# Kernel tuning notes

Measured on AMD Instinct MI355X. Metric: run time of the kernel, lower is better.

## Reference

```python
import jax, jax.numpy as jnp
import numpy as np

B, T, D = 2, 2048, 2048
H, HD = 16, 128          # n_heads, head_dim
K, L = 4, 24             # n_bases, total_layers
FF = D * 1               # ff_mult = 1 (required by route_down dim match)


def setup_inputs() -> dict:
    key = jax.random.key(0)
    ks = jax.random.split(key, 16)
    s = jnp.float32(0.02)
    bias_base = jnp.zeros((L, K), jnp.float32).at[:, 0].set(5.0)
    return {
        "x": jax.random.normal(ks[0], (B, T, D), jnp.float32),
        "gamma": jnp.ones((D,), jnp.float32),
        "beta": jnp.zeros((D,), jnp.float32),
        "iter_scale": jnp.ones((), jnp.float32),
        "qkv_bases": jax.random.normal(ks[1], (K, 3 * D, D), jnp.float32) * s,
        "o_bases": jax.random.normal(ks[2], (K, D, D), jnp.float32) * s,
        "gate_bases": jax.random.normal(ks[3], (K, FF, D), jnp.float32) * s,
        "up_bases": jax.random.normal(ks[4], (K, FF, D), jnp.float32) * s,
        "down_bases": jax.random.normal(ks[5], (K, D, FF), jnp.float32) * s,
        "route_qkv": jax.random.normal(ks[6], (L, K, D), jnp.float32) * s,
        "route_o": jax.random.normal(ks[7], (L, K, D), jnp.float32) * s,
        "route_gate": jax.random.normal(ks[8], (L, K, D), jnp.float32) * s,
        "route_up": jax.random.normal(ks[9], (L, K, D), jnp.float32) * s,
        "route_down": jax.random.normal(ks[10], (L, K, FF), jnp.float32) * s,
        "bias_qkv": bias_base + 0.1 * jax.random.normal(ks[11], (L, K), jnp.float32),
        "bias_o": bias_base + 0.1 * jax.random.normal(ks[12], (L, K), jnp.float32),
        "bias_gate": bias_base + 0.1 * jax.random.normal(ks[13], (L, K), jnp.float32),
        "bias_up": bias_base + 0.1 * jax.random.normal(ks[14], (L, K), jnp.float32),
        "bias_down": bias_base + 0.1 * jax.random.normal(ks[15], (L, K), jnp.float32),
        "norm1_w": jnp.ones((D,), jnp.float32),
        "norm2_w": jnp.ones((D,), jnp.float32),
        "layer_idx": 5,
    }


def _rmsnorm(x, w):
    eps = jnp.finfo(x.dtype).eps  # nn.RMSNorm default eps
    return x * jax.lax.rsqrt(jnp.mean(x * x, axis=-1, keepdims=True) + eps) * w


def _mixed_linear(x, bases, route_l, bias_l):
    # route_l: (K, d_in), bias_l: (K,) for this layer
    logits = jnp.einsum('btd,kd->btk', x, route_l) / jnp.sqrt(jnp.float32(D)) + bias_l
    alpha = jax.nn.softmax(logits, axis=-1)                    # (B,T,K)
    y = jnp.einsum('btk,kod,btd->bto', alpha, bases, x)        # weighted combine of K linears
    return y, alpha


def reference(x, gamma, beta, iter_scale, qkv_bases, o_bases, gate_bases, up_bases,
              down_bases, route_qkv, route_o, route_gate, route_up, route_down,
              bias_qkv, bias_o, bias_gate, bias_up, bias_down, norm1_w, norm2_w, layer_idx):
    li = layer_idx
    h = _rmsnorm(x, norm1_w) * gamma + beta
    qkv, a_qkv = _mixed_linear(h, qkv_bases, route_qkv[li], bias_qkv[li])
    qkv = qkv.reshape(B, T, 3, H, HD).transpose(2, 0, 3, 1, 4)  # (3,B,H,T,HD)
    q, k, v = qkv[0], qkv[1], qkv[2]
    scores = jnp.einsum('bhqd,bhkd->bhqk', q, k) / jnp.sqrt(jnp.float32(HD))
    causal = jnp.triu(jnp.ones((T, T), bool), 1)
    scores = jnp.where(causal, -jnp.inf, scores)
    attn = jax.nn.softmax(scores, axis=-1)
    out = jnp.einsum('bhqk,bhkd->bhqd', attn, v).transpose(0, 2, 1, 3).reshape(B, T, D)
    attn_out, _ = _mixed_linear(out, o_bases, route_o[li], bias_o[li])
    x_attn = x + attn_out
    h2 = _rmsnorm(x_attn, norm2_w) * gamma + beta
    gate_out, _ = _mixed_linear(h2, gate_bases, route_gate[li], bias_gate[li])
    up_out, _ = _mixed_linear(h2, up_bases, route_up[li], bias_up[li])
    ffn_in = jax.nn.silu(gate_out) * up_out
    down_out, _ = _mixed_linear(ffn_in, down_bases, route_down[li], bias_down[li])
    x_ffn = x_attn + down_out
    return x + (x_ffn - x) * iter_scale, a_qkv
```

## Files before the change

kernel.cpp:

```cpp
#include <hip/hip_runtime.h>


typedef __attribute__((ext_vector_type(8))) short short8;
typedef __attribute__((ext_vector_type(4))) float f32x4;
typedef __attribute__((ext_vector_type(4))) unsigned uint4_t;

#define BT 4096
#define DD 2048
#define KD 8192
#define NH 16
#define HD_ 128
#define RSCALE 0.02209708691207961f
#define ASCALE 0.08838834764831845f

__device__ inline float bf2f(short s) {
  return __uint_as_float(((unsigned)(unsigned short)s) << 16);
}
__device__ inline short f2bf(float f) {
  unsigned u = __float_as_uint(f);
  u += 0x7FFFu + ((u >> 16) & 1u);
  return (short)(u >> 16);
}
__device__ inline f32x4 zero4() { f32x4 v; v[0]=0.f; v[1]=0.f; v[2]=0.f; v[3]=0.f; return v; }

__device__ inline void async_copy16(const void* g, void* l) {
  __builtin_amdgcn_global_load_lds(
      (const __attribute__((address_space(1))) unsigned*)g,
      (__attribute__((address_space(3))) unsigned*)l, 16, 0, 0);
}

__global__ __launch_bounds__(256)
void cvt_bf16_kernel(const float* __restrict__ in, short* __restrict__ out,
                     const int nchunk) {
  const int i = blockIdx.x * 256 + threadIdx.x;
  if (i >= nchunk) return;
  const float* p = in + (size_t)i * 8;
  float4 u0 = *(const float4*)p;
  float4 u1 = *(const float4*)(p + 4);
  uint4_t pk;
  pk[0] = __builtin_amdgcn_perm(__float_as_uint(u0.y), __float_as_uint(u0.x), 0x07060302);
  pk[1] = __builtin_amdgcn_perm(__float_as_uint(u0.w), __float_as_uint(u0.z), 0x07060302);
  pk[2] = __builtin_amdgcn_perm(__float_as_uint(u1.y), __float_as_uint(u1.x), 0x07060302);
  pk[3] = __builtin_amdgcn_perm(__float_as_uint(u1.w), __float_as_uint(u1.z), 0x07060302);
  *(uint4_t*)(out + (size_t)i * 8) = pk;
}

__global__ __launch_bounds__(256)
void rmsnorm_kernel(const float* __restrict__ x, const float* __restrict__ w,
                    const float* __restrict__ gamma, const float* __restrict__ beta,
                    short* __restrict__ out) {
  const int t = blockIdx.x;
  const float* xr = x + (size_t)t * DD;
  const int base = threadIdx.x * 8;
  float4 v0 = *(const float4*)(xr + base);
  float4 v1 = *(const float4*)(xr + base + 4);
  float ss = v0.x*v0.x + v0.y*v0.y + v0.z*v0.z + v0.w*v0.w
           + v1.x*v1.x + v1.y*v1.y + v1.z*v1.z + v1.w*v1.w;
  #pragma unroll
  for (int off = 32; off > 0; off >>= 1) ss += __shfl_xor(ss, off, 64);
  __shared__ float red[4];
  const int lane = threadIdx.x & 63, wv = threadIdx.x >> 6;
  if (lane == 0) red[wv] = ss;
  __syncthreads();
  const float tot = red[0] + red[1] + red[2] + red[3];
  const float inv = rsqrtf(tot * (1.0f / DD) + 1.1920929e-07f);
  float xv[8] = {v0.x,v0.y,v0.z,v0.w,v1.x,v1.y,v1.z,v1.w};
  short8 o;
  #pragma unroll
  for (int j = 0; j < 8; ++j)
    o[j] = f2bf(xv[j] * inv * w[base+j] * gamma[base+j] + beta[base+j]);
  *(short8*)(out + (size_t)t * DD + base) = o;
}

__global__ __launch_bounds__(64)
void route_kernel(const short* __restrict__ in,
                  const float* __restrict__ routeB,
                  const float* __restrict__ biasB,
                  const int* __restrict__ li_ptr,
                  float* __restrict__ alpha,
                  float* __restrict__ aout)
{
  const int t = blockIdx.x;
  const int lane = threadIdx.x;
  const int li = *li_ptr;
  const float* R = routeB + (size_t)li * 4 * DD;
  const float* bias = biasB + li * 4;
  const short* xr = in + (size_t)t * DD;
  float acc0 = 0.f, acc1 = 0.f, acc2 = 0.f, acc3 = 0.f;
  for (int i = lane; i < DD; i += 64) {
    float v = bf2f(xr[i]);
    acc0 += v * R[i];
    acc1 += v * R[DD + i];
    acc2 += v * R[2*DD + i];
    acc3 += v * R[3*DD + i];
  }
  #pragma unroll
  for (int off = 32; off > 0; off >>= 1) {
    acc0 += __shfl_xor(acc0, off, 64);
    acc1 += __shfl_xor(acc1, off, 64);
    acc2 += __shfl_xor(acc2, off, 64);
    acc3 += __shfl_xor(acc3, off, 64);
  }
  if (lane == 0) {
    float lg[4] = {acc0 * RSCALE + bias[0], acc1 * RSCALE + bias[1],
                   acc2 * RSCALE + bias[2], acc3 * RSCALE + bias[3]};
    float mx = fmaxf(fmaxf(lg[0], lg[1]), fmaxf(lg[2], lg[3]));
    float se = 0.f;
    #pragma unroll
    for (int k = 0; k < 4; ++k) { lg[k] = __expf(lg[k] - mx); se += lg[k]; }
    const float rinv = 1.0f / se;
    #pragma unroll
    for (int k = 0; k < 4; ++k) {
      float a = lg[k] * rinv;
      alpha[(size_t)t*4 + k] = a;
      if (aout) aout[(size_t)t*4 + k] = a;
    }
  }
}

__global__ __launch_bounds__(256)
void expand_kernel(const short* __restrict__ in, const float* __restrict__ alpha,
                   short* __restrict__ out)
{
  const int t = blockIdx.x;
  const short* hr = in + (size_t)t * DD;
  const float a0 = alpha[(size_t)t*4], a1 = alpha[(size_t)t*4+1],
              a2 = alpha[(size_t)t*4+2], a3 = alpha[(size_t)t*4+3];
  const float av[4] = {a0, a1, a2, a3};
  #pragma unroll
  for (int c = 0; c < 4; ++c) {
    int ci = threadIdx.x + 256 * c;
    int kk = ci * 8;
    int kidx = kk >> 11;
    int d = kk & 2047;
    short8 v = *(const short8*)(hr + d);
    float s = av[kidx];
    short8 o;
    #pragma unroll
    for (int j = 0; j < 8; ++j) o[j] = f2bf(bf2f(v[j]) * s);
    *(short8*)(out + (size_t)t * KD + kk) = o;
  }
}

__global__ __launch_bounds__(256)
void gemm_qkv(const short* __restrict__ Aexp,
              const short* __restrict__ Bwb,
              short* __restrict__ outp)
{
  __shared__ __align__(16) short As[128*64];
  __shared__ __align__(16) short Bs[128*64];
  const int tid = threadIdx.x;
  const int lane = tid & 63, wave = tid >> 6;
  const int lr = lane & 15, lg = lane >> 4;
  const int wm = (wave & 1) * 64, wn = (wave >> 1) * 64;
  const int m0 = blockIdx.y * 128, n0 = blockIdx.x * 128;

  f32x4 acc[4][4];
  #pragma unroll
  for (int i = 0; i < 4; ++i)
    #pragma unroll
    for (int j = 0; j < 4; ++j) acc[i][j] = zero4();

  const int srow = tid >> 3, sc8 = tid & 7;
  const short* Ab = Aexp + (size_t)(m0 + srow) * KD + sc8 * 8;
  const short* Bb = Bwb + (size_t)(n0 + srow) * DD + sc8 * 8;

  for (int kt = 0; kt < 128; ++kt) {
    const int kk0 = kt << 6;
    const int kidx = kk0 >> 11;
    const int dbase = kk0 & 2047;
    #pragma unroll
    for (int c = 0; c < 4; ++c) {
      const int i = tid + 256 * c;
      async_copy16(Ab + (size_t)(c * 32) * KD + kk0, As + i * 8);
      async_copy16(Bb + ((size_t)kidx * 6144 + c * 32) * DD + dbase, Bs + i * 8);
    }
    __syncthreads();
    #pragma unroll
    for (int s = 0; s < 2; ++s) {
      short8 af[4], bfr[4];
      #pragma unroll
      for (int i = 0; i < 4; ++i) af[i]  = *(const short8*)(As + (wm + i*16 + lr)*64 + s*32 + lg*8);
      #pragma unroll
      for (int j = 0; j < 4; ++j) bfr[j] = *(const short8*)(Bs + (wn + j*16 + lr)*64 + s*32 + lg*8);
      #pragma unroll
      for (int i = 0; i < 4; ++i)
        #pragma unroll
        for (int j = 0; j < 4; ++j)
          acc[i][j] = __builtin_amdgcn_mfma_f32_16x16x32_bf16(af[i], bfr[j], acc[i][j], 0, 0, 0);
    }
    __syncthreads();
  }
  #pragma unroll
  for (int i = 0; i < 4; ++i) {
    #pragma unroll
    for (int r = 0; r < 4; ++r) {
      const int m = m0 + wm + i*16 + lg*4 + r;
      #pragma unroll
      for (int j = 0; j < 4; ++j) {
        const int n = n0 + wn + j*16 + lr;
        outp[(size_t)m * 6144 + n] = f2bf(acc[i][j][r]);
      }
    }
  }
}

__global__ __launch_bounds__(256)
void gemm_wide(const short* __restrict__ A,
               const short* __restrict__ Bc,
               short* __restrict__ Z)
{
  __shared__ __align__(16) short As[128*64];
  __shared__ __align__(16) short Bs[128*64];
  const int tid = threadIdx.x;
  const int lane = tid & 63, wave = tid >> 6;
  const int lr = lane & 15, lg = lane >> 4;
  const int wm = (wave & 1) * 64, wn = (wave >> 1) * 64;
  const int m0 = blockIdx.y * 128, n0 = blockIdx.x * 128;

  f32x4 acc[4][4];
  #pragma unroll
  for (int i = 0; i < 4; ++i)
    #pragma unroll
    for (int j = 0; j < 4; ++j) acc[i][j] = zero4();

  const int srow = tid >> 3, sc8 = tid & 7;
  const short* Ab = A  + (size_t)(m0 + srow) * DD + sc8 * 8;
  const short* Bb = Bc + (size_t)(n0 + srow) * DD + sc8 * 8;

  for (int kt = 0; kt < 32; ++kt) {
    const int kk0 = kt << 6;
    #pragma unroll
    for (int c = 0; c < 4; ++c) {
      const int i = tid + 256 * c;
      async_copy16(Ab + (size_t)(c * 32) * DD + kk0, As + i * 8);
      async_copy16(Bb + (size_t)(c * 32) * DD + kk0, Bs + i * 8);
    }
    __syncthreads();
    #pragma unroll
    for (int s = 0; s < 2; ++s) {
      short8 af[4], bfr[4];
      #pragma unroll
      for (int i = 0; i < 4; ++i) af[i]  = *(const short8*)(As + (wm + i*16 + lr)*64 + s*32 + lg*8);
      #pragma unroll
      for (int j = 0; j < 4; ++j) bfr[j] = *(const short8*)(Bs + (wn + j*16 + lr)*64 + s*32 + lg*8);
      #pragma unroll
      for (int i = 0; i < 4; ++i)
        #pragma unroll
        for (int j = 0; j < 4; ++j)
          acc[i][j] = __builtin_amdgcn_mfma_f32_16x16x32_bf16(af[i], bfr[j], acc[i][j], 0, 0, 0);
    }
    __syncthreads();
  }
  #pragma unroll
  for (int i = 0; i < 4; ++i) {
    #pragma unroll
    for (int r = 0; r < 4; ++r) {
      const int m = m0 + wm + i*16 + lg*4 + r;
      #pragma unroll
      for (int j = 0; j < 4; ++j) {
        const int n = n0 + wn + j*16 + lr;
        Z[(size_t)m * 8192 + n] = f2bf(acc[i][j][r]);
      }
    }
  }
}

__global__ __launch_bounds__(256)
void combine_kernel(const short* __restrict__ Z,
                    const float* __restrict__ alpha,
                    const int mode,
                    const float* __restrict__ x,
                    const float* __restrict__ xattn,
                    const float* __restrict__ iter_s,
                    const short* __restrict__ gate,
                    void* __restrict__ outp)
{
  const int t = blockIdx.x;
  const int d0 = threadIdx.x * 8;
  const float a0 = alpha[(size_t)t*4],   a1 = alpha[(size_t)t*4+1],
              a2 = alpha[(size_t)t*4+2], a3 = alpha[(size_t)t*4+3];
  const short* zr = Z + (size_t)t * 8192 + d0;
  short8 z0 = *(const short8*)(zr);
  short8 z1 = *(const short8*)(zr + 2048);
  short8 z2 = *(const short8*)(zr + 4096);
  short8 z3 = *(const short8*)(zr + 6144);
  float y[8];
  #pragma unroll
  for (int j = 0; j < 8; ++j)
    y[j] = a0*bf2f(z0[j]) + a1*bf2f(z1[j]) + a2*bf2f(z2[j]) + a3*bf2f(z3[j]);
  const size_t base = (size_t)t * DD + d0;
  if (mode == 0) {
    short8 o;
    #pragma unroll
    for (int j = 0; j < 8; ++j) o[j] = f2bf(y[j]);
    *(short8*)((short*)outp + base) = o;
  } else if (mode == 1) {
    float4 x0 = *(const float4*)(x + base);
    float4 x1 = *(const float4*)(x + base + 4);
    float xv[8] = {x0.x,x0.y,x0.z,x0.w,x1.x,x1.y,x1.z,x1.w};
    float* op = (float*)outp;
    #pragma unroll
    for (int j = 0; j < 8; ++j) op[base + j] = xv[j] + y[j];
  } else if (mode == 2) {
    short8 gv = *(const short8*)(gate + base);
    short8 o;
    #pragma unroll
    for (int j = 0; j < 8; ++j) {
      float xg = bf2f(gv[j]);
      float s = xg / (1.0f + __expf(-xg));
      o[j] = f2bf(s * y[j]);
    }
    *(short8*)((short*)outp + base) = o;
  } else {
    const float is = *iter_s;
    float4 x0 = *(const float4*)(x + base);
    float4 x1 = *(const float4*)(x + base + 4);
    float4 t0 = *(const float4*)(xattn + base);
    float4 t1 = *(const float4*)(xattn + base + 4);
    float xv[8] = {x0.x,x0.y,x0.z,x0.w,x1.x,x1.y,x1.z,x1.w};
    float tv[8] = {t0.x,t0.y,t0.z,t0.w,t1.x,t1.y,t1.z,t1.w};
    float* op = (float*)outp;
    #pragma unroll
    for (int j = 0; j < 8; ++j) op[base + j] = xv[j] + (tv[j] + y[j] - xv[j]) * is;
  }
}

__global__ __launch_bounds__(256)
void transpose_v_kernel(const short* __restrict__ qkv, short* __restrict__ vt)
{
  __shared__ __align__(16) short tile[64][72];
  const int t0 = blockIdx.x * 64;
  const int hd0 = blockIdx.y * 64;
  const int bh = blockIdx.z;
  const int b = bh >> 4, h = bh & 15;
  const int tid = threadIdx.x;
  #pragma unroll
  for (int c = 0; c < 2; ++c) {
    int ci = tid + 256 * c;
    int tr = ci >> 3, c8 = ci & 7;
    *(short8*)&tile[tr][c8*8] =
      *(const short8*)(qkv + (size_t)(b*2048 + t0 + tr)*6144 + 4096 + h*HD_ + hd0 + c8*8);
  }
  __syncthreads();
  #pragma unroll
  for (int c = 0; c < 2; ++c) {
    int ci = tid + 256 * c;
    int hr = ci >> 3, c8 = ci & 7;
    short8 o;
    #pragma unroll
    for (int j = 0; j < 8; ++j) o[j] = tile[c8*8 + j][hr];
    *(short8*)(vt + (size_t)(bh*HD_ + hd0 + hr)*2048 + t0 + c8*8) = o;
  }
}

__global__ __launch_bounds__(256, 2)
void attn_kernel(const short* __restrict__ qkv,
                 const short* __restrict__ vt,
                 short* __restrict__ attnout)
{
  __shared__ __align__(16) short Ks[32][136];
  __shared__ __align__(16) short Vt[128][40];
  __shared__ __align__(16) short Ps[4][16][40];
  const int bid = blockIdx.x;
  const int qt = bid & 31, bh = bid >> 5;
  const int b = bh >> 4, h = bh & 15;
  const int q0 = qt * 64;
  const int tid = threadIdx.x, lane = tid & 63, w = tid >> 6;
  const int lr = lane & 15, lg = lane >> 4;
  const int q0w = q0 + w * 16;

  short8 qf[4];
  {
    const size_t qbase = (size_t)(b*2048 + q0w + lr) * 6144 + h * HD_;
    #pragma unroll
    for (int s = 0; s < 4; ++s)
      qf[s] = *(const short8*)(qkv + qbase + s*32 + lg*8);
  }
  float m_run[4], l_run[4];
  f32x4 acc[8];
  #pragma unroll
  for (int r = 0; r < 4; ++r) { m_run[r] = -1e30f; l_run[r] = 0.f; }
  #pragma unroll
  for (int dt = 0; dt < 8; ++dt) acc[dt] = zero4();

  const int ntiles = (q0 + 64) >> 5;
  for (int jt = 0; jt < ntiles; ++jt) {
    const int j0 = jt << 5;
    #pragma unroll
    for (int c = 0; c < 2; ++c) {
      int ci = tid + 256 * c;
      int key = ci >> 4, hd8 = ci & 15;
      *(short8*)&Ks[key][hd8*8] =
        *(const short8*)(qkv + (size_t)(b*2048 + j0 + key)*6144 + 2048 + h*HD_ + hd8*8);
    }
    #pragma unroll
    for (int c = 0; c < 2; ++c) {
      int ci = tid + 256 * c;
      int hd = ci >> 2, k8 = ci & 3;
      *(short8*)&Vt[hd][k8*8] =
        *(const short8*)(vt + (size_t)(bh*HD_ + hd)*2048 + j0 + k8*8);
    }
    __syncthreads();
    f32x4 sc0 = zero4(), sc1 = zero4();
    #pragma unroll
    for (int s = 0; s < 4; ++s) {
      short8 kb0 = *(const short8*)&Ks[lr][s*32 + lg*8];
      short8 kb1 = *(const short8*)&Ks[16 + lr][s*32 + lg*8];
      sc0 = __builtin_amdgcn_mfma_f32_16x16x32_bf16(qf[s], kb0, sc0, 0, 0, 0);
      sc1 = __builtin_amdgcn_mfma_f32_16x16x32_bf16(qf[s], kb1, sc1, 0, 0, 0);
    }
    float pv0[4], pv1[4], al[4];
    #pragma unroll
    for (int r = 0; r < 4; ++r) {
      const int q = q0w + lg*4 + r;
      float v0 = sc0[r] * ASCALE; if (j0 + lr > q)      v0 = -1e30f;
      float v1 = sc1[r] * ASCALE; if (j0 + 16 + lr > q) v1 = -1e30f;
      float mx = fmaxf(v0, v1);
      mx = fmaxf(mx, __shfl_xor(mx, 1, 16));
      mx = fmaxf(mx, __shfl_xor(mx, 2, 16));
      mx = fmaxf(mx, __shfl_xor(mx, 4, 16));
      mx = fmaxf(mx, __shfl_xor(mx, 8, 16));
      const float mnew = fmaxf(m_run[r], mx);
      const float a = __expf(m_run[r] - mnew);
      v0 = __expf(v0 - mnew);
      v1 = __expf(v1 - mnew);
      float rs = v0 + v1;
      rs += __shfl_xor(rs, 1, 16);
      rs += __shfl_xor(rs, 2, 16);
      rs += __shfl_xor(rs, 4, 16);
      rs += __shfl_xor(rs, 8, 16);
      l_run[r] = l_run[r] * a + rs;
      m_run[r] = mnew;
      al[r] = a; pv0[r] = v0; pv1[r] = v1;
    }
    #pragma unroll
    for (int dt = 0; dt < 8; ++dt)
      #pragma unroll
      for (int r = 0; r < 4; ++r) acc[dt][r] *= al[r];
    #pragma unroll
    for (int r = 0; r < 4; ++r) {
      Ps[w][lg*4 + r][lr]      = f2bf(pv0[r]);
      Ps[w][lg*4 + r][16 + lr] = f2bf(pv1[r]);
    }
    short8 pa = *(const short8*)&Ps[w][lr][lg*8];
    #pragma unroll
    for (int dt = 0; dt < 8; ++dt) {
      short8 vb = *(const short8*)&Vt[dt*16 + lr][lg*8];
      acc[dt] = __builtin_amdgcn_mfma_f32_16x16x32_bf16(pa, vb, acc[dt], 0, 0, 0);
    }
    __syncthreads();
  }
  #pragma unroll
  for (int dt = 0; dt < 8; ++dt) {
    #pragma unroll
    for (int r = 0; r < 4; ++r) {
      const int q = q0w + lg*4 + r;
      attnout[(size_t)(b*2048 + q)*2048 + h*HD_ + dt*16 + lr] = f2bf(acc[dt][r] / l_run[r]);
    }
  }
}

extern "C" void kernel_launch(void* const* d_in, const int* in_sizes, int n_in,
                              void* d_out, int out_size, void* d_ws, size_t ws_size,
                              hipStream_t stream) {
  const float* x          = (const float*)d_in[0];
  const float* gamma      = (const float*)d_in[1];
  const float* beta       = (const float*)d_in[2];
  const float* iter_scale = (const float*)d_in[3];
  const float* qkv_bases  = (const float*)d_in[4];
  const float* o_bases    = (const float*)d_in[5];
  const float* gate_bases = (const float*)d_in[6];
  const float* up_bases   = (const float*)d_in[7];
  const float* down_bases = (const float*)d_in[8];
  const float* route_qkv  = (const float*)d_in[9];
  const float* route_o    = (const float*)d_in[10];
  const float* route_gate = (const float*)d_in[11];
  const float* route_up   = (const float*)d_in[12];
  const float* route_down = (const float*)d_in[13];
  const float* bias_qkv   = (const float*)d_in[14];
  const float* bias_o     = (const float*)d_in[15];
  const float* bias_gate  = (const float*)d_in[16];
  const float* bias_up    = (const float*)d_in[17];
  const float* bias_down  = (const float*)d_in[18];
  const float* norm1_w    = (const float*)d_in[19];
  const float* norm2_w    = (const float*)d_in[20];
  const int*   li         = (const int*)d_in[21];

  float* out0 = (float*)d_out;
  float* aout = out0 + (size_t)BT * DD;

  char* ws = (char*)d_ws;
  short* hbuf    = (short*)(ws + 0);
  float* alpha   = (float*)(ws + 16777216);
  short* Zbuf    = (short*)(ws + 16842752);
  short* Bconv   = (short*)(ws + 83951616);
  short* qkvbuf  = (short*)(ws + 184614912);
  short* vtbuf   = (short*)(ws + 234946560);
  short* attnout = (short*)(ws + 251723776);
  float* x_attn  = (float*)(ws + 184614912);
  short* gatebuf = (short*)(ws + 218169344);

  const int NCH_QKV = 50331648 / 8;
  const int NCH_D   = 16777216 / 8;

  rmsnorm_kernel<<<BT, 256, 0, stream>>>(x, norm1_w, gamma, beta, hbuf);
  cvt_bf16_kernel<<<NCH_QKV/256, 256, 0, stream>>>(qkv_bases, Bconv, NCH_QKV);
  route_kernel<<<BT, 64, 0, stream>>>(hbuf, route_qkv, bias_qkv, li, alpha, aout);
  expand_kernel<<<BT, 256, 0, stream>>>(hbuf, alpha, Zbuf);
  gemm_qkv<<<dim3(48, 32), 256, 0, stream>>>(Zbuf, Bconv, qkvbuf);
  transpose_v_kernel<<<dim3(32, 2, 32), 256, 0, stream>>>(qkvbuf, vtbuf);
  attn_kernel<<<1024, 256, 0, stream>>>(qkvbuf, vtbuf, attnout);
  cvt_bf16_kernel<<<NCH_D/256, 256, 0, stream>>>(o_bases, Bconv, NCH_D);
  route_kernel<<<BT, 64, 0, stream>>>(attnout, route_o, bias_o, li, alpha, nullptr);
  gemm_wide<<<dim3(64, 32), 256, 0, stream>>>(attnout, Bconv, Zbuf);
  combine_kernel<<<BT, 256, 0, stream>>>(Zbuf, alpha, 1, x, nullptr, nullptr,
                                         nullptr, x_attn);
  rmsnorm_kernel<<<BT, 256, 0, stream>>>(x_attn, norm2_w, gamma, beta, hbuf);
  cvt_bf16_kernel<<<NCH_D/256, 256, 0, stream>>>(gate_bases, Bconv, NCH_D);
  route_kernel<<<BT, 64, 0, stream>>>(hbuf, route_gate, bias_gate, li, alpha, nullptr);
  gemm_wide<<<dim3(64, 32), 256, 0, stream>>>(hbuf, Bconv, Zbuf);
  combine_kernel<<<BT, 256, 0, stream>>>(Zbuf, alpha, 0, nullptr, nullptr, nullptr,
                                         nullptr, gatebuf);
  cvt_bf16_kernel<<<NCH_D/256, 256, 0, stream>>>(up_bases, Bconv, NCH_D);
  route_kernel<<<BT, 64, 0, stream>>>(hbuf, route_up, bias_up, li, alpha, nullptr);
  gemm_wide<<<dim3(64, 32), 256, 0, stream>>>(hbuf, Bconv, Zbuf);
  combine_kernel<<<BT, 256, 0, stream>>>(Zbuf, alpha, 2, nullptr, nullptr, nullptr,
                                         gatebuf, gatebuf);
  cvt_bf16_kernel<<<NCH_D/256, 256, 0, stream>>>(down_bases, Bconv, NCH_D);
  route_kernel<<<BT, 64, 0, stream>>>(gatebuf, route_down, bias_down, li, alpha, nullptr);
  gemm_wide<<<dim3(64, 32), 256, 0, stream>>>(gatebuf, Bconv, Zbuf);
  combine_kernel<<<BT, 256, 0, stream>>>(Zbuf, alpha, 3, x, x_attn, iter_scale,
                                         nullptr, out0);
}
```

Baseline: 1.996 ms.

## Replace GEMMs with 256x256-tile triple-buffered swizzled 8-wave MFMA kernel

Replaces the two 128x128 single-buffered GEMM kernels with one templated 512-thread kernel. It uses 256x256 output tiles and a 3-stage async-copy LDS ring with explicit vmcnt waits. An XOR swizzle on the LDS layout avoids bank conflicts, and setprio is raised around the MFMA block. The aim is to overlap global loads with compute, raise data reuse per tile and cut LDS conflicts. In exchange it uses more registers (32 accumulators per wave) and launches fewer blocks, which may hurt occupancy and tail balance.

```diff
diff --git a/kernel.cpp b/kernel.cpp
--- a/kernel.cpp
+++ b/kernel.cpp
@@ -142,128 +142,99 @@
   }
 }
 
-__global__ __launch_bounds__(256)
-void gemm_qkv(const short* __restrict__ Aexp,
-              const short* __restrict__ Bwb,
-              short* __restrict__ outp)
+__global__ __launch_bounds__(512)
+void gemm8p_qkv(const short* __restrict__ A, const short* __restrict__ B,
+                short* __restrict__ C);
+
+template<bool QKV, int AST, int KTOT, int NST>
+__global__ __launch_bounds__(512)
+void gemm8p(const short* __restrict__ A, const short* __restrict__ B,
+            short* __restrict__ C)
 {
-  __shared__ __align__(16) short As[128*64];
-  __shared__ __align__(16) short Bs[128*64];
+  constexpr int NS = KTOT / 32;
+  __shared__ __align__(16) short As[3][256 * 32];
+  __shared__ __align__(16) short Bs[3][256 * 32];
   const int tid = threadIdx.x;
   const int lane = tid & 63, wave = tid >> 6;
   const int lr = lane & 15, lg = lane >> 4;
-  const int wm = (wave & 1) * 64, wn = (wave >> 1) * 64;
-  const int m0 = blockIdx.y * 128, n0 = blockIdx.x * 128;
-
-  f32x4 acc[4][4];
-  #pragma unroll
-  for (int i = 0; i < 4; ++i)
+  const int wm = wave >> 2, wn = wave & 3;
+  const int m0 = blockIdx.y * 256, n0 = blockIdx.x * 256;
+
+  const int srow = tid >> 2;
+  const int pc = (tid & 3) ^ ((tid >> 3) & 3);
+  const short* Aab = A + (size_t)(m0 + srow) * AST + pc * 8;
+  const short* Bab = B + (size_t)(n0 + srow) * 2048 + pc * 8;
+
+  f32x4 acc[8][4];
+  #pragma unroll
+  for (int i = 0; i < 8; ++i)
     #pragma unroll
     for (int j = 0; j < 4; ++j) acc[i][j] = zero4();
 
-  const int srow = tid >> 3, sc8 = tid & 7;
-  const short* Ab = Aexp + (size_t)(m0 + srow) * KD + sc8 * 8;
-  const short* Bb = Bwb + (size_t)(n0 + srow) * DD + sc8 * 8;
-
-  for (int kt = 0; kt < 128; ++kt) {
-    const int kk0 = kt << 6;
-    const int kidx = kk0 >> 11;
-    const int dbase = kk0 & 2047;
-    #pragma unroll
-    for (int c = 0; c < 4; ++c) {
-      const int i = tid + 256 * c;
-      async_copy16(Ab + (size_t)(c * 32) * KD + kk0, As + i * 8);
-      async_copy16(Bb + ((size_t)kidx * 6144 + c * 32) * DD + dbase, Bs + i * 8);
-    }
-    __syncthreads();
-    #pragma unroll
-    for (int s = 0; s < 2; ++s) {
-      short8 af[4], bfr[4];
+  auto stage = [&](int ks_) {
+    const int b_ = ks_ % 3;
+    short* la = &As[b_][0] + tid * 8;
+    short* lb = &Bs[b_][0] + tid * 8;
+    if constexpr (QKV) {
+      const int kidx = ks_ >> 6;
+      const int dbase = (ks_ & 63) * 32;
+      const short* as_ = Aab + ks_ * 32;
+      const short* bs_ = Bab + (size_t)kidx * (6144 * 2048) + dbase;
+      async_copy16(as_, la);
+      async_copy16(as_ + 128 * AST, la + 4096);
+      async_copy16(bs_, lb);
+      async_copy16(bs_ + 128 * 2048, lb + 4096);
+    } else {
+      const int k0 = ks_ * 32;
+      async_copy16(Aab + k0, la);
+      async_copy16(Aab + k0 + 128 * AST, la + 4096);
+      async_copy16(Bab + k0, lb);
+      async_copy16(Bab + k0 + 128 * 2048, lb + 4096);
+    }
+  };
+
+  stage(0); stage(1); stage(2);
+
+  const int acol = (lg ^ ((lr >> 1) & 3)) * 8;
+
+  for (int ks = 0; ks < NS; ++ks) {
+    const int b = ks % 3;
+    const int rem = NS - 1 - ks;
+    if (rem >= 2)      asm volatile("s_waitcnt vmcnt(8)" ::: "memory");
+    else if (rem == 1) asm volatile("s_waitcnt vmcnt(4)" ::: "memory");
+    else               asm volatile("s_waitcnt vmcnt(0)" ::: "memory");
+    __builtin_amdgcn_s_barrier();
+    short8 af[8], bg[4];
+    const short* ap = &As[b][0] + (wm * 128 + lr) * 32 + acol;
+    #pragma unroll
+    for (int i = 0; i < 8; ++i) af[i] = *(const short8*)(ap + i * 512);
+    const short* bp = &Bs[b][0] + (wn * 64 + lr) * 32 + acol;
+    #pragma unroll
+    for (int j = 0; j < 4; ++j) bg[j] = *(const short8*)(bp + j * 512);
+    asm volatile("s_waitcnt lgkmcnt(0)" ::: "memory");
+    __builtin_amdgcn_sched_barrier(0);
+    __builtin_amdgcn_s_setprio(1);
+    #pragma unroll
+    for (int i = 0; i < 8; ++i)
       #pragma unroll
-      for (int i = 0; i < 4; ++i) af[i]  = *(const short8*)(As + (wm + i*16 + lr)*64 + s*32 + lg*8);
-      #pragma unroll
-      for (int j = 0; j < 4; ++j) bfr[j] = *(const short8*)(Bs + (wn + j*16 + lr)*64 + s*32 + lg*8);
-      #pragma unroll
-      for (int i = 0; i < 4; ++i)
-        #pragma unroll
-        for (int j = 0; j < 4; ++j)
-          acc[i][j] = __builtin_amdgcn_mfma_f32_16x16x32_bf16(af[i], bfr[j], acc[i][j], 0, 0, 0);
-    }
-    __syncthreads();
-  }
-  #pragma unroll
-  for (int i = 0; i < 4; ++i) {
+      for (int j = 0; j < 4; ++j)
+        acc[i][j] = __builtin_amdgcn_mfma_f32_16x16x32_bf16(af[i], bg[j], acc[i][j], 0, 0, 0);
+    __builtin_amdgcn_s_setprio(0);
+    __builtin_amdgcn_s_barrier();
+    if (ks + 3 < NS) stage(ks + 3);
+  }
+
+  #pragma unroll
+  for (int i = 0; i < 8; ++i)
     #pragma unroll
     for (int r = 0; r < 4; ++r) {
-      const int m = m0 + wm + i*16 + lg*4 + r;
+      const int m = m0 + wm * 128 + i * 16 + lg * 4 + r;
       #pragma unroll
       for (int j = 0; j < 4; ++j) {
-        const int n = n0 + wn + j*16 + lr;
-        outp[(size_t)m * 6144 + n] = f2bf(acc[i][j][r]);
+        const int n = n0 + wn * 64 + j * 16 + lr;
+        C[(size_t)m * NST + n] = f2bf(acc[i][j][r]);
       }
     }
-  }
-}
-
-__global__ __launch_bounds__(256)
-void gemm_wide(const short* __restrict__ A,
-               const short* __restrict__ Bc,
-               short* __restrict__ Z)
-{
-  __shared__ __align__(16) short As[128*64];
-  __shared__ __align__(16) short Bs[128*64];
-  const int tid = threadIdx.x;
-  const int lane = tid & 63, wave = tid >> 6;
-  const int lr = lane & 15, lg = lane >> 4;
-  const int wm = (wave & 1) * 64, wn = (wave >> 1) * 64;
-  const int m0 = blockIdx.y * 128, n0 = blockIdx.x * 128;
-
-  f32x4 acc[4][4];
-  #pragma unroll
-  for (int i = 0; i < 4; ++i)
-    #pragma unroll
-    for (int j = 0; j < 4; ++j) acc[i][j] = zero4();
-
-  const int srow = tid >> 3, sc8 = tid & 7;
-  const short* Ab = A  + (size_t)(m0 + srow) * DD + sc8 * 8;
-  const short* Bb = Bc + (size_t)(n0 + srow) * DD + sc8 * 8;
-
-  for (int kt = 0; kt < 32; ++kt) {
-    const int kk0 = kt << 6;
-    #pragma unroll
-    for (int c = 0; c < 4; ++c) {
-      const int i = tid + 256 * c;
-      async_copy16(Ab + (size_t)(c * 32) * DD + kk0, As + i * 8);
-      async_copy16(Bb + (size_t)(c * 32) * DD + kk0, Bs + i * 8);
-    }
-    __syncthreads();
-    #pragma unroll
-    for (int s = 0; s < 2; ++s) {
-      short8 af[4], bfr[4];
-      #pragma unroll
-      for (int i = 0; i < 4; ++i) af[i]  = *(const short8*)(As + (wm + i*16 + lr)*64 + s*32 + lg*8);
-      #pragma unroll
-      for (int j = 0; j < 4; ++j) bfr[j] = *(const short8*)(Bs + (wn + j*16 + lr)*64 + s*32 + lg*8);
-      #pragma unroll
-      for (int i = 0; i < 4; ++i)
-        #pragma unroll
-        for (int j = 0; j < 4; ++j)
-          acc[i][j] = __builtin_amdgcn_mfma_f32_16x16x32_bf16(af[i], bfr[j], acc[i][j], 0, 0, 0);
-    }
-    __syncthreads();
-  }
-  #pragma unroll
-  for (int i = 0; i < 4; ++i) {
-    #pragma unroll
-    for (int r = 0; r < 4; ++r) {
-      const int m = m0 + wm + i*16 + lg*4 + r;
-      #pragma unroll
-      for (int j = 0; j < 4; ++j) {
-        const int n = n0 + wn + j*16 + lr;
-        Z[(size_t)m * 8192 + n] = f2bf(acc[i][j][r]);
-      }
-    }
-  }
 }
 
 __global__ __launch_bounds__(256)
@@ -508,28 +479,28 @@
   cvt_bf16_kernel<<<NCH_QKV/256, 256, 0, stream>>>(qkv_bases, Bconv, NCH_QKV);
   route_kernel<<<BT, 64, 0, stream>>>(hbuf, route_qkv, bias_qkv, li, alpha, aout);
   expand_kernel<<<BT, 256, 0, stream>>>(hbuf, alpha, Zbuf);
-  gemm_qkv<<<dim3(48, 32), 256, 0, stream>>>(Zbuf, Bconv, qkvbuf);
+  gemm8p<true, 8192, 8192, 6144><<<dim3(24, 16), 512, 0, stream>>>(Zbuf, Bconv, qkvbuf);
   transpose_v_kernel<<<dim3(32, 2, 32), 256, 0, stream>>>(qkvbuf, vtbuf);
   attn_kernel<<<1024, 256, 0, stream>>>(qkvbuf, vtbuf, attnout);
   cvt_bf16_kernel<<<NCH_D/256, 256, 0, stream>>>(o_bases, Bconv, NCH_D);
   route_kernel<<<BT, 64, 0, stream>>>(attnout, route_o, bias_o, li, alpha, nullptr);
-  gemm_wide<<<dim3(64, 32), 256, 0, stream>>>(attnout, Bconv, Zbuf);
+  gemm8p<false, 2048, 2048, 8192><<<dim3(32, 16), 512, 0, stream>>>(attnout, Bconv, Zbuf);
   combine_kernel<<<BT, 256, 0, stream>>>(Zbuf, alpha, 1, x, nullptr, nullptr,
                                          nullptr, x_attn);
   rmsnorm_kernel<<<BT, 256, 0, stream>>>(x_attn, norm2_w, gamma, beta, hbuf);
   cvt_bf16_kernel<<<NCH_D/256, 256, 0, stream>>>(gate_bases, Bconv, NCH_D);
   route_kernel<<<BT, 64, 0, stream>>>(hbuf, route_gate, bias_gate, li, alpha, nullptr);
-  gemm_wide<<<dim3(64, 32), 256, 0, stream>>>(hbuf, Bconv, Zbuf);
+  gemm8p<false, 2048, 2048, 8192><<<dim3(32, 16), 512, 0, stream>>>(hbuf, Bconv, Zbuf);
   combine_kernel<<<BT, 256, 0, stream>>>(Zbuf, alpha, 0, nullptr, nullptr, nullptr,
                                          nullptr, gatebuf);
   cvt_bf16_kernel<<<NCH_D/256, 256, 0, stream>>>(up_bases, Bconv, NCH_D);
   route_kernel<<<BT, 64, 0, stream>>>(hbuf, route_up, bias_up, li, alpha, nullptr);
-  gemm_wide<<<dim3(64, 32), 256, 0, stream>>>(hbuf, Bconv, Zbuf);
+  gemm8p<false, 2048, 2048, 8192><<<dim3(32, 16), 512, 0, stream>>>(hbuf, Bconv, Zbuf);
   combine_kernel<<<BT, 256, 0, stream>>>(Zbuf, alpha, 2, nullptr, nullptr, nullptr,
                                          gatebuf, gatebuf);
   cvt_bf16_kernel<<<NCH_D/256, 256, 0, stream>>>(down_bases, Bconv, NCH_D);
   route_kernel<<<BT, 64, 0, stream>>>(gatebuf, route_down, bias_down, li, alpha, nullptr);
-  gemm_wide<<<dim3(64, 32), 256, 0, stream>>>(gatebuf, Bconv, Zbuf);
+  gemm8p<false, 2048, 2048, 8192><<<dim3(32, 16), 512, 0, stream>>>(gatebuf, Bconv, Zbuf);
   combine_kernel<<<BT, 256, 0, stream>>>(Zbuf, alpha, 3, x, x_attn, iter_scale,
                                          nullptr, out0);
 }
```

Measured after the change: 2.116 ms. 1.06x slower.
